# Kernel tuning notes

Hardware: AMD Instinct MI355X
Metric: run time of the kernel (lower is better)

The kernel has to match this reference:

```python
import jax, jax.numpy as jnp
import numpy as np

B, S, HID = 2, 2048, 2048
NH = 16
HD = HID // NH  # 128


def setup_inputs() -> dict:
    key = jax.random.key(0)
    ks = jax.random.split(key, 12)
    sc = 0.02
    return {
        "hidden_state": jax.random.normal(ks[0], (B, S, HID), jnp.float32),
        "attention_mask": jax.random.uniform(ks[1], (B, 1, S, S), jnp.float32),
        "Wq": jax.random.normal(ks[2], (HID, HID), jnp.float32) * sc,
        "bq": jnp.zeros((HID,), jnp.float32),
        "Wk": jax.random.normal(ks[3], (HD, HID), jnp.float32) * sc,
        "bk": jnp.zeros((HD,), jnp.float32),
        "Wv": jax.random.normal(ks[4], (HD, HID), jnp.float32) * sc,
        "bv": jnp.zeros((HD,), jnp.float32),
        "Wo": jax.random.normal(ks[5], (HID, HID), jnp.float32) * sc,
        "bo": jnp.zeros((HID,), jnp.float32),
    }


def reference(hidden_state, attention_mask, Wq, bq, Wk, bk, Wv, bv, Wo, bo):
    b = hidden_state.shape[0]
    # projections (nn.Linear: x @ W.T + b)
    q = hidden_state @ Wq.T + bq                      # [B,S,HID]
    k = hidden_state @ Wk.T + bk                      # [B,S,HD] (single shared head)
    v = hidden_state @ Wv.T + bv                      # [B,S,HD]
    # split heads: q -> [B,NH,S,HD]
    q = q.reshape(b, -1, NH, HD).transpose(0, 2, 1, 3)
    scale = jnp.sqrt(jnp.asarray(HD, q.dtype))
    scores = jnp.einsum('bhsd,btd->bhst', q, k) / scale  # [B,NH,S,S]
    # faithful to source: mask scaled by -1e-09 (as written)
    scores = scores + attention_mask * (-1e-09)
    probs = jax.nn.softmax(scores, axis=-1)
    out = jnp.einsum('bhst,btd->bhsd', probs, v)          # [B,NH,S,HD]
    # faithful to source: transpose(-1,-2) then flat view to [B,S,HID]
    out = out.transpose(0, 1, 3, 2).reshape(b, -1, HD * NH)
    return out @ Wo.T + bo
```

## Files before the change

### kernel.cpp

```cpp
#include <hip/hip_runtime.h>
#include <hip/hip_bf16.h>

#define BATCH 2
#define SEQ 2048
#define HIDDIM 2048
#define NHEADS 16
#define HDIM 128
#define QKVN 2304

typedef __attribute__((ext_vector_type(8))) short bf16x8;
typedef __attribute__((ext_vector_type(4))) short short4v;
typedef __attribute__((ext_vector_type(4))) float f32x4;
typedef __attribute__((ext_vector_type(16))) float f32x16;
typedef __attribute__((ext_vector_type(4))) unsigned u32x4;

__device__ __forceinline__ short f2bf(float f) {
  unsigned u = __builtin_bit_cast(unsigned, f);
  unsigned r = (u + 0x7fffu + ((u >> 16) & 1u)) >> 16;
  return (short)r;
}

__device__ __forceinline__ unsigned cvtpk_bf16(float a, float b) {
  unsigned r;
  asm("v_cvt_pk_bf16_f32 %0, %1, %2" : "=v"(r) : "v"(a), "v"(b));
  return r;
}

#define PLSWAP(a, b) asm("v_permlane32_swap_b32 %0, %1" : "+v"(a), "+v"(b))

__device__ __forceinline__ void gl_lds16(const void* g, void* l) {
  __builtin_amdgcn_global_load_lds(
      (const __attribute__((address_space(1))) void*)g,
      (__attribute__((address_space(3))) void*)l, 16, 0, 0);
}

__device__ __forceinline__ float max3f(float a, float b, float c) {
  return fmaxf(fmaxf(a, b), c);
}
__device__ __forceinline__ float vmax16(const f32x16& v) {
  float a = max3f(v[0], v[1], v[2]);
  float b = max3f(v[3], v[4], v[5]);
  float c = max3f(v[6], v[7], v[8]);
  float d = max3f(v[9], v[10], v[11]);
  float e = max3f(v[12], v[13], v[14]);
  return fmaxf(max3f(a, b, c), max3f(d, e, v[15]));
}

__global__ void prep_kernel(const float* __restrict__ h, const float* __restrict__ Wq,
                            const float* __restrict__ Wk, const float* __restrict__ Wv,
                            const float* __restrict__ Wo,
                            const float* __restrict__ bq, const float* __restrict__ bk,
                            const float* __restrict__ bv,
                            short* __restrict__ h_bf, short* __restrict__ Wqkv_bf,
                            short* __restrict__ Wo_bf, float* __restrict__ bqkv)
{
  int bid = blockIdx.x;
  const float* src;
  short* dst;
  int n;
  if (bid < 8192)        { src = h;  dst = h_bf;                n = 8388608; }
  else if (bid < 12288)  { src = Wq; dst = Wqkv_bf;             n = 4194304; bid -= 8192; }
  else if (bid < 12544)  { src = Wk; dst = Wqkv_bf + 4194304;   n = 262144;  bid -= 12288; }
  else if (bid < 12800)  { src = Wv; dst = Wqkv_bf + 4456448;   n = 262144;  bid -= 12544; }
  else if (bid < 12809) {
    int i = (bid - 12800) * 256 + threadIdx.x;
    if (i < QKVN) {
      float v;
      if (i < HIDDIM) v = bq[i];
      else if (i < HIDDIM + HDIM) v = bk[i - HIDDIM];
      else v = bv[i - HIDDIM - HDIM];
      bqkv[i] = v;
    }
    return;
  }
  else                   { src = Wo; dst = Wo_bf;               n = 4194304; bid -= 12809; }
  int i = (bid * 256 + threadIdx.x) * 4;
  if (i >= n) return;
  float4 v = *(const float4*)(src + i);
  short4v o;
  o[0] = f2bf(v.x); o[1] = f2bf(v.y); o[2] = f2bf(v.z); o[3] = f2bf(v.w);
  *(short4v*)(dst + i) = o;
}

__global__ void cvt_kernel(const float* __restrict__ in, short* __restrict__ out, int n) {
  int i = (blockIdx.x * blockDim.x + threadIdx.x) * 4;
  if (i >= n) return;
  float4 v = *(const float4*)(in + i);
  short4v o;
  o[0] = f2bf(v.x); o[1] = f2bf(v.y); o[2] = f2bf(v.z); o[3] = f2bf(v.w);
  *(short4v*)(out + i) = o;
}

template <int MODE>
__global__ __launch_bounds__(256, 3)
void gemm_bt(const short* __restrict__ A, const short* __restrict__ W,
             const float* __restrict__ bias, void* __restrict__ Cv, void* __restrict__ Cv2,
             int M, int N, int K)
{
  __shared__ short As[128 * 64];
  __shared__ short Ws[128 * 64];
  const int tid = threadIdx.x;
  const int lane = tid & 63;
  const int w = tid >> 6;
  const int wr = w >> 1, wc = w & 1;

  const int gx = gridDim.x;
  const int nwg = gx * gridDim.y;
  const int id = blockIdx.y * gx + blockIdx.x;
  const int cpx = nwg >> 3;
  const int swz = (id & 7) * cpx + (id >> 3);
  const int tn = (swz % gx) * 128, tm = (swz / gx) * 128;

  const int rA = lane & 15;
  const int r7 = rA & 7;
  const int srow = lane >> 3;
  const int scg  = (lane & 7) ^ srow;

  f32x4 acc[4][4] = {};

  for (int k0 = 0; k0 < K; k0 += 64) {
    __syncthreads();
#pragma unroll
    for (int i = 0; i < 4; ++i) {
      int ch = w * 4 + i;
      gl_lds16(A + (size_t)(tm + ch * 8 + srow) * K + k0 + scg * 8, As + ch * 512);
      gl_lds16(W + (size_t)(tn + ch * 8 + srow) * K + k0 + scg * 8, Ws + ch * 512);
    }
    __syncthreads();
#pragma unroll
    for (int kk = 0; kk < 64; kk += 32) {
      const int cg = (kk >> 3) + (lane >> 4);
      const int co = ((cg ^ r7) << 3);
      bf16x8 af[4];
#pragma unroll
      for (int mi = 0; mi < 4; ++mi)
        af[mi] = *(const bf16x8*)(As + ((wr * 64 + mi * 16 + rA) << 6) + co);
#pragma unroll
      for (int ni = 0; ni < 4; ++ni) {
        bf16x8 wf = *(const bf16x8*)(Ws + ((wc * 64 + ni * 16 + rA) << 6) + co);
#pragma unroll
        for (int mi = 0; mi < 4; ++mi)
          acc[mi][ni] = __builtin_amdgcn_mfma_f32_16x16x32_bf16(af[mi], wf, acc[mi][ni], 0, 0, 0);
      }
    }
  }

  const float QSCALE = 0.12752600954427384f;
  const int cr = (lane >> 4) * 4;
  const int cc = lane & 15;
#pragma unroll
  for (int ni = 0; ni < 4; ++ni) {
    int col = tn + wc * 64 + ni * 16 + cc;
    float bv = bias[col];
#pragma unroll
    for (int mi = 0; mi < 4; ++mi) {
#pragma unroll
      for (int r = 0; r < 4; ++r) {
        int row = tm + wr * 64 + mi * 16 + cr + r;
        float v = acc[mi][ni][r] + bv;
        if constexpr (MODE == 0) {
          ((float*)Cv)[(size_t)row * N + col] = v;
        } else {
          if (col < HIDDIM)
            ((short*)Cv)[(size_t)row * QKVN + col] = f2bf(v * QSCALE);
          else if (col < HIDDIM + HDIM)
            ((short*)Cv)[(size_t)row * QKVN + col] = f2bf(v);
          else
            ((short*)Cv2)[(size_t)(col - HIDDIM - HDIM) * (BATCH * SEQ) + row] = f2bf(v);
        }
      }
    }
  }
}

__global__ __launch_bounds__(512, 2)
void attn_kernel(const short* __restrict__ QKV, const short* __restrict__ Vt,
                 short* __restrict__ OT)
{
  __shared__ short smem[2][32768];
  const int tid = threadIdx.x;
  const int l31 = tid & 31;
  const int hi2 = (tid >> 5) & 1;
  const int w = tid >> 6;
  const int b = blockIdx.z, h = blockIdx.y, qt = blockIdx.x;
  const int rx = l31 & 15;
  const short* Kp = QKV + HIDDIM;

  const short* kptr[4];
  const short* vptr[4];
  {
    const int rin = (tid & 63) >> 4;
    const int gp = tid & 15;
#pragma unroll
    for (int i = 0; i < 4; ++i) {
      int ch = w * 4 + i;
      int row = ch * 4 + rin;
      int gl = gp ^ (row & 15);
      kptr[i] = Kp + (size_t)(b * SEQ + row) * QKVN + gl * 8;
      vptr[i] = Vt + (size_t)row * (BATCH * SEQ) + b * SEQ + gl * 8;
    }
  }

  bf16x8 qf[8];
  {
    const short* Qp = QKV + (size_t)(b * SEQ + qt * 256 + w * 32 + l31) * QKVN + h * HDIM;
#pragma unroll
    for (int kk = 0; kk < 8; ++kk)
      qf[kk] = *(const bf16x8*)(Qp + kk * 16 + hi2 * 8);
  }

  f32x16 o[4] = {};
  float m = -1e30f, l = 0.f;

#pragma unroll
  for (int i = 0; i < 4; ++i) {
    int ch = w * 4 + i;
    gl_lds16(kptr[i], (short*)smem[0] + ch * 512);
    gl_lds16(vptr[i], (short*)smem[0] + 16384 + ch * 512);
    kptr[i] += 128 * QKVN;
    vptr[i] += 128;
  }
  __syncthreads();

  for (int c = 0; c < 16; ++c) {
    const short* Ks = smem[c & 1];
    const short* Vs = smem[c & 1] + 16384;
    if (c < 15) {
      short* nb = smem[(c + 1) & 1];
#pragma unroll
      for (int i = 0; i < 4; ++i) {
        int ch = w * 4 + i;
        gl_lds16(kptr[i], nb + ch * 512);
        gl_lds16(vptr[i], nb + 16384 + ch * 512);
        kptr[i] += 128 * QKVN;
        vptr[i] += 128;
      }
    }

    f32x16 s[4] = {};
    __builtin_amdgcn_s_setprio(1);
#pragma unroll
    for (int n = 0; n < 4; ++n) {
      const int row = n * 32 + l31;
      bf16x8 kf[8];
#pragma unroll
      for (int kk = 0; kk < 8; ++kk)
        kf[kk] = *(const bf16x8*)(Ks + row * 128 + (((kk * 2 + hi2) ^ rx) << 3));
#pragma unroll
      for (int kk = 0; kk < 8; ++kk)
        s[n] = __builtin_amdgcn_mfma_f32_32x32x16_bf16(kf[kk], qf[kk], s[n], 0, 0, 0);
    }
    __builtin_amdgcn_s_setprio(0);

    float mx = fmaxf(fmaxf(vmax16(s[0]), vmax16(s[1])),
                     fmaxf(vmax16(s[2]), vmax16(s[3])));
    mx = fmaxf(mx, __shfl_xor(mx, 32));
    if (!__all(mx <= m + 8.f)) {
      float mn = fmaxf(m, mx);
      float cf = __builtin_amdgcn_exp2f(m - mn);
      m = mn; l *= cf;
#pragma unroll
      for (int nd = 0; nd < 4; ++nd)
#pragma unroll
        for (int r = 0; r < 16; ++r) o[nd][r] *= cf;
    }

    float rs = 0.f;
#pragma unroll
    for (int n = 0; n < 4; ++n) {
      float p[16];
#pragma unroll
      for (int r = 0; r < 16; ++r)
        p[r] = __builtin_amdgcn_exp2f(s[n][r] - m);
      rs += (((p[0] + p[1]) + (p[2] + p[3])) + ((p[4] + p[5]) + (p[6] + p[7])))
          + (((p[8] + p[9]) + (p[10] + p[11])) + ((p[12] + p[13]) + (p[14] + p[15])));
      unsigned w0 = cvtpk_bf16(p[0], p[1]),  w1 = cvtpk_bf16(p[2], p[3]);
      unsigned w2 = cvtpk_bf16(p[4], p[5]),  w3 = cvtpk_bf16(p[6], p[7]);
      unsigned w4 = cvtpk_bf16(p[8], p[9]),  w5 = cvtpk_bf16(p[10], p[11]);
      unsigned w6 = cvtpk_bf16(p[12], p[13]), w7 = cvtpk_bf16(p[14], p[15]);
      PLSWAP(w0, w2); PLSWAP(w1, w3);
      PLSWAP(w4, w6); PLSWAP(w5, w7);
      bf16x8 pa0 = __builtin_bit_cast(bf16x8, (u32x4){w0, w1, w2, w3});
      bf16x8 pa1 = __builtin_bit_cast(bf16x8, (u32x4){w4, w5, w6, w7});
      bf16x8 vf[8];
#pragma unroll
      for (int nd = 0; nd < 4; ++nd) {
        const int row = nd * 32 + l31;
        vf[nd * 2]     = *(const bf16x8*)(Vs + row * 128 + ((((n * 2) * 2 + hi2) ^ rx) << 3));
        vf[nd * 2 + 1] = *(const bf16x8*)(Vs + row * 128 + ((((n * 2 + 1) * 2 + hi2) ^ rx) << 3));
      }
      __builtin_amdgcn_s_setprio(1);
#pragma unroll
      for (int nd = 0; nd < 4; ++nd) {
        o[nd] = __builtin_amdgcn_mfma_f32_32x32x16_bf16(vf[nd * 2], pa0, o[nd], 0, 0, 0);
        o[nd] = __builtin_amdgcn_mfma_f32_32x32x16_bf16(vf[nd * 2 + 1], pa1, o[nd], 0, 0, 0);
      }
      __builtin_amdgcn_s_setprio(0);
    }
    rs += __shfl_xor(rs, 32);
    l += rs;
    __syncthreads();
  }

  const float inv = 1.f / l;
  short* dst = OT + (size_t)b * (SEQ * HIDDIM) + (size_t)(h * HDIM) * SEQ
             + qt * 256 + w * 32 + l31;
#pragma unroll
  for (int nd = 0; nd < 4; ++nd) {
#pragma unroll
    for (int r = 0; r < 16; ++r) {
      int d = nd * 32 + (r & 3) + 8 * (r >> 2) + 4 * hi2;
      dst[(size_t)d * SEQ] = f2bf(o[nd][r] * inv);
    }
  }
}

extern "C" void kernel_launch(void* const* d_in, const int* in_sizes, int n_in,
                              void* d_out, int out_size, void* d_ws, size_t ws_size,
                              hipStream_t stream)
{
  const float* hidden = (const float*)d_in[0];
  const float* Wq = (const float*)d_in[2];
  const float* bq = (const float*)d_in[3];
  const float* Wk = (const float*)d_in[4];
  const float* bk = (const float*)d_in[5];
  const float* Wv = (const float*)d_in[6];
  const float* bv = (const float*)d_in[7];
  const float* Wo = (const float*)d_in[8];
  const float* bo = (const float*)d_in[9];
  float* out = (float*)d_out;

  short* ws      = (short*)d_ws;
  short* QKV     = ws;
  short* Vt_bf   = ws + 9437184;
  short* h_bf    = Vt_bf + 524288;
  short* OT      = h_bf;
  short* Wqkv_bf = h_bf + 8388608;
  float* bqkv    = (float*)(Wqkv_bf + 4718592);
  short* Wo_sep  = (short*)(bqkv + QKVN);

  const bool sep = ws_size >= (size_t)54535168;
  short* Wo_bf = sep ? Wo_sep : QKV;

  prep_kernel<<<sep ? 16905 : 12809, 256, 0, stream>>>(
      hidden, Wq, Wk, Wv, Wo, bq, bk, bv, h_bf, Wqkv_bf, Wo_bf, bqkv);

  gemm_bt<3><<<dim3(18, 32, 1), 256, 0, stream>>>(h_bf, Wqkv_bf, bqkv, QKV, Vt_bf,
                                                  4096, QKVN, 2048);
  attn_kernel<<<dim3(8, 16, 2), 512, 0, stream>>>(QKV, Vt_bf, OT);
  if (!sep) cvt_kernel<<<4096, 256, 0, stream>>>(Wo, Wo_bf, 4194304);
  gemm_bt<0><<<dim3(16, 32, 1), 256, 0, stream>>>(OT, Wo_bf, bo, out, nullptr,
                                                  4096, 2048, 2048);
}
```

Before: 178.6 us.

## Shrink attention tiles to 128 queries and 64-key chunks with 256 threads

The attention kernel now runs 256-thread blocks covering 128 query rows each, so twice as many blocks launch. KV chunks drop from 128 to 64 keys, which halves LDS use per block. The V tile staging and fragment addressing are rewritten to fit the new 64-key layout. The aim is more blocks per CU and better occupancy and load balance, at the cost of reloading K/V from global memory for twice as many query tiles and running twice as many barrier iterations.

After: 183.8 us. +2.9%, slower.

```diff
diff --git a/kernel.cpp b/kernel.cpp
--- a/kernel.cpp
+++ b/kernel.cpp
@@ -173,11 +173,11 @@
   }
 }
 
-__global__ __launch_bounds__(512, 2)
+__global__ __launch_bounds__(256, 2)
 void attn_kernel(const short* __restrict__ QKV, const short* __restrict__ Vt,
                  short* __restrict__ OT)
 {
-  __shared__ short smem[2][32768];
+  __shared__ short smem[2][16384];
   const int tid = threadIdx.x;
   const int l31 = tid & 31;
   const int hi2 = (tid >> 5) & 1;
@@ -186,24 +186,24 @@
   const int rx = l31 & 15;
   const short* Kp = QKV + HIDDIM;
 
-  const short* kptr[4];
-  const short* vptr[4];
+  const short* kp[4];
+  const short* vp[4];
   {
-    const int rin = (tid & 63) >> 4;
-    const int gp = tid & 15;
 #pragma unroll
     for (int i = 0; i < 4; ++i) {
-      int ch = w * 4 + i;
-      int row = ch * 4 + rin;
-      int gl = gp ^ (row & 15);
-      kptr[i] = Kp + (size_t)(b * SEQ + row) * QKVN + gl * 8;
-      vptr[i] = Vt + (size_t)row * (BATCH * SEQ) + b * SEQ + gl * 8;
+      int s = tid + 256 * i;
+      int r = s >> 4;
+      int g = (s & 15) ^ (r & 15);
+      kp[i] = Kp + (size_t)(b * SEQ + r) * QKVN + g * 8;
+      int d = (g >> 3) * 64 + r;
+      int e = g & 7;
+      vp[i] = Vt + (size_t)d * (BATCH * SEQ) + b * SEQ + e * 8;
     }
   }
 
   bf16x8 qf[8];
   {
-    const short* Qp = QKV + (size_t)(b * SEQ + qt * 256 + w * 32 + l31) * QKVN + h * HDIM;
+    const short* Qp = QKV + (size_t)(b * SEQ + qt * 128 + w * 32 + l31) * QKVN + h * HDIM;
 #pragma unroll
     for (int kk = 0; kk < 8; ++kk)
       qf[kk] = *(const bf16x8*)(Qp + kk * 16 + hi2 * 8);
@@ -212,35 +212,27 @@
   f32x16 o[4] = {};
   float m = -1e30f, l = 0.f;
 
-#pragma unroll
-  for (int i = 0; i < 4; ++i) {
-    int ch = w * 4 + i;
-    gl_lds16(kptr[i], (short*)smem[0] + ch * 512);
-    gl_lds16(vptr[i], (short*)smem[0] + 16384 + ch * 512);
-    kptr[i] += 128 * QKVN;
-    vptr[i] += 128;
-  }
+#define STAGE(BUF)                                                          \
+  { short* nb = (short*)smem[BUF];                                          \
+    _Pragma("unroll")                                                       \
+    for (int i = 0; i < 4; ++i) {                                           \
+      gl_lds16(kp[i], nb + (w * 64 + 256 * i) * 8);                         \
+      gl_lds16(vp[i], nb + 8192 + (w * 64 + 256 * i) * 8);                  \
+      kp[i] += 64 * QKVN; vp[i] += 64;                                      \
+    } }
+
+  STAGE(0);
   __syncthreads();
 
-  for (int c = 0; c < 16; ++c) {
+  for (int c = 0; c < 32; ++c) {
     const short* Ks = smem[c & 1];
-    const short* Vs = smem[c & 1] + 16384;
-    if (c < 15) {
-      short* nb = smem[(c + 1) & 1];
-#pragma unroll
-      for (int i = 0; i < 4; ++i) {
-        int ch = w * 4 + i;
-        gl_lds16(kptr[i], nb + ch * 512);
-        gl_lds16(vptr[i], nb + 16384 + ch * 512);
-        kptr[i] += 128 * QKVN;
-        vptr[i] += 128;
-      }
-    }
-
-    f32x16 s[4] = {};
+    const short* Vs = smem[c & 1] + 8192;
+    if (c < 31) STAGE((c + 1) & 1);
+
+    f32x16 s2[2] = {};
     __builtin_amdgcn_s_setprio(1);
 #pragma unroll
-    for (int n = 0; n < 4; ++n) {
+    for (int n = 0; n < 2; ++n) {
       const int row = n * 32 + l31;
       bf16x8 kf[8];
 #pragma unroll
@@ -248,12 +240,11 @@
         kf[kk] = *(const bf16x8*)(Ks + row * 128 + (((kk * 2 + hi2) ^ rx) << 3));
 #pragma unroll
       for (int kk = 0; kk < 8; ++kk)
-        s[n] = __builtin_amdgcn_mfma_f32_32x32x16_bf16(kf[kk], qf[kk], s[n], 0, 0, 0);
+        s2[n] = __builtin_amdgcn_mfma_f32_32x32x16_bf16(kf[kk], qf[kk], s2[n], 0, 0, 0);
     }
     __builtin_amdgcn_s_setprio(0);
 
-    float mx = fmaxf(fmaxf(vmax16(s[0]), vmax16(s[1])),
-                     fmaxf(vmax16(s[2]), vmax16(s[3])));
+    float mx = fmaxf(vmax16(s2[0]), vmax16(s2[1]));
     mx = fmaxf(mx, __shfl_xor(mx, 32));
     if (!__all(mx <= m + 8.f)) {
       float mn = fmaxf(m, mx);
@@ -267,11 +258,11 @@
 
     float rs = 0.f;
 #pragma unroll
-    for (int n = 0; n < 4; ++n) {
+    for (int n = 0; n < 2; ++n) {
       float p[16];
 #pragma unroll
       for (int r = 0; r < 16; ++r)
-        p[r] = __builtin_amdgcn_exp2f(s[n][r] - m);
+        p[r] = __builtin_amdgcn_exp2f(s2[n][r] - m);
       rs += (((p[0] + p[1]) + (p[2] + p[3])) + ((p[4] + p[5]) + (p[6] + p[7])))
           + (((p[8] + p[9]) + (p[10] + p[11])) + ((p[12] + p[13]) + (p[14] + p[15])));
       unsigned w0 = cvtpk_bf16(p[0], p[1]),  w1 = cvtpk_bf16(p[2], p[3]);
@@ -285,9 +276,12 @@
       bf16x8 vf[8];
 #pragma unroll
       for (int nd = 0; nd < 4; ++nd) {
-        const int row = nd * 32 + l31;
-        vf[nd * 2]     = *(const bf16x8*)(Vs + row * 128 + ((((n * 2) * 2 + hi2) ^ rx) << 3));
-        vf[nd * 2 + 1] = *(const bf16x8*)(Vs + row * 128 + ((((n * 2 + 1) * 2 + hi2) ^ rx) << 3));
+        const int r2 = (nd & 1) * 32 + l31;
+        const int ph = (nd >> 1) * 8;
+        vf[nd * 2]     = *(const bf16x8*)(Vs + r2 * 128 +
+                          (((ph + (n * 2) * 2 + hi2) ^ rx) << 3));
+        vf[nd * 2 + 1] = *(const bf16x8*)(Vs + r2 * 128 +
+                          (((ph + (n * 2 + 1) * 2 + hi2) ^ rx) << 3));
       }
       __builtin_amdgcn_s_setprio(1);
 #pragma unroll
@@ -301,10 +295,11 @@
     l += rs;
     __syncthreads();
   }
+#undef STAGE
 
   const float inv = 1.f / l;
   short* dst = OT + (size_t)b * (SEQ * HIDDIM) + (size_t)(h * HDIM) * SEQ
-             + qt * 256 + w * 32 + l31;
+             + qt * 128 + w * 32 + l31;
 #pragma unroll
   for (int nd = 0; nd < 4; ++nd) {
 #pragma unroll
@@ -347,7 +342,7 @@
 
   gemm_bt<3><<<dim3(18, 32, 1), 256, 0, stream>>>(h_bf, Wqkv_bf, bqkv, QKV, Vt_bf,
                                                   4096, QKVN, 2048);
-  attn_kernel<<<dim3(8, 16, 2), 512, 0, stream>>>(QKV, Vt_bf, OT);
+  attn_kernel<<<dim3(16, 16, 2), 256, 0, stream>>>(QKV, Vt_bf, OT);
   if (!sep) cvt_kernel<<<4096, 256, 0, stream>>>(Wo, Wo_bf, 4194304);
   gemm_bt<0><<<dim3(16, 32, 1), 256, 0, stream>>>(OT, Wo_bf, bo, out, nullptr,
                                                   4096, 2048, 2048);
```
